# Performance work log

Hardware: AMD Instinct MI355X
Metric: run time of the kernel (lower is better)

The kernel has to match this reference:

```python
import jax, jax.numpy as jnp
import numpy as np
from jax import lax

FORGET_BIAS = 1.0
EPS = 1e-12


def l2_normalize_time(x):
    # tf.nn.l2_normalize(x, dim=1): normalize over the timestep axis
    sq = jnp.sum(jnp.square(x), axis=1, keepdims=True)
    return x * lax.rsqrt(jnp.maximum(sq, EPS))


def lstm_layer(x, W, b, units):
    """TF LSTMCell: kernel (in+units, 4*units), gates split as i, j, f, o.
    x: [B, T, D] -> [B, T, units]"""
    B = x.shape[0]

    def step(carry, xt):
        c, h = carry
        z = jnp.concatenate([xt, h], axis=-1) @ W + b  # [B, 4*units]
        i, j, f, o = jnp.split(z, 4, axis=-1)
        c = jax.nn.sigmoid(f + FORGET_BIAS) * c + jax.nn.sigmoid(i) * jnp.tanh(j)
        h = jax.nn.sigmoid(o) * jnp.tanh(c)
        return (c, h), h

    init = (jnp.zeros((B, units), x.dtype), jnp.zeros((B, units), x.dtype))
    _, hs = lax.scan(step, init, jnp.swapaxes(x, 0, 1))  # [T, B, units]
    return jnp.swapaxes(hs, 0, 1)


def setup_inputs() -> dict:
    key = jax.random.key(0)
    ks = jax.random.split(key, 5)
    B, T, U = 256, 2048, 64
    x = jax.random.normal(ks[0], (B, T, 1), dtype=jnp.float32)
    # layer 0: LSTMCell(64), input dim 1 -> kernel (1+64, 4*64)
    W0 = jax.random.normal(ks[1], (1 + U, 4 * U), dtype=jnp.float32) * 0.05
    b0 = jnp.zeros((4 * U,), dtype=jnp.float32)
    # layer 1: LSTMCell(1), input dim 64 -> kernel (64+1, 4)
    W1 = jax.random.normal(ks[2], (U + 1, 4), dtype=jnp.float32) * 0.05
    b1 = jnp.zeros((4,), dtype=jnp.float32)
    # dense(1)
    Wd = jax.random.normal(ks[3], (1, 1), dtype=jnp.float32)
    bd = jnp.zeros((1,), dtype=jnp.float32)
    return {"x": x, "W0": W0, "b0": b0, "W1": W1, "b1": b1, "Wd": Wd, "bd": bd}


def reference(x, W0, b0, W1, b1, Wd, bd):
    h = l2_normalize_time(x)          # [B, T, 1]
    h = lstm_layer(h, W0, b0, 64)     # [B, T, 64]
    h = lstm_layer(h, W1, b1, 1)      # [B, T, 1]
    out = h @ Wd + bd                 # dense(1), no activation
    return out
```

## Files before the change

### kernel.cpp

```cpp
#include <hip/hip_runtime.h>
#include <math.h>

#define TT 2048
#define UU 64
#define BB 256
#define NTHR 320

typedef float v2f __attribute__((ext_vector_type(2)));
typedef float v4f __attribute__((ext_vector_type(4)));

__device__ __forceinline__ float frcp(float x) { return __builtin_amdgcn_rcpf(x); }
__device__ __forceinline__ float fsigmoid(float x) { return frcp(1.0f + __expf(-x)); }
__device__ __forceinline__ float ftanh(float x) { return 1.0f - 2.0f * frcp(1.0f + __expf(2.0f * x)); }

__device__ __forceinline__ void pkfma(v2f& a, v2f h, v2f w) {
    asm("v_pk_fma_f32 %0, %1, %2, %0" : "+v"(a) : "v"(h), "v"(w));
}

__global__
__attribute__((amdgpu_flat_work_group_size(NTHR, NTHR)))
__attribute__((amdgpu_waves_per_eu(1, 2)))
void lstm_ts_kernel(
    const float* __restrict__ x, const float* __restrict__ W0,
    const float* __restrict__ b0, const float* __restrict__ W1,
    const float* __restrict__ b1, const float* __restrict__ Wd,
    const float* __restrict__ bd, float* __restrict__ out)
{
    __shared__ __align__(16) float xbuf[TT];
    __shared__ __align__(16) float ringP[4][2][UU];
    __shared__ __align__(16) float zbuf[4 * UU];
    __shared__ float red[5];

    const int tid = threadIdx.x;
    const int wid = tid >> 6;
    const int u = tid & 63;
    const int b = blockIdx.x;
    const float* xrow = x + b * TT;
    float* outrow = out + b * TT;

    float ss = 0.f;
    for (int i = tid; i < TT; i += NTHR) {
        float v = xrow[i];
        xbuf[i] = v;
        ss += v * v;
    }
    #pragma unroll
    for (int m = 1; m < 64; m <<= 1) ss += __shfl_xor(ss, m, 64);
    if (u == 0) red[wid] = ss;
    if (wid < 4) ringP[wid][1][u] = 0.f;
    __syncthreads();

    if (wid < 4) {
        const int g = wid;
        const int c = g * 64 + u;
        const float sq = ((red[0] + red[1]) + (red[2] + red[3])) + red[4];
        const float scale = 1.0f / sqrtf(fmaxf(sq, 1e-12f));

        #define DECLW(m) v2f WP##m; { const float* r_ = W0 + (1 + 2*(m)) * 256 + c; \
            WP##m.x = r_[0]; WP##m.y = r_[256]; } \
            asm volatile("" : "+v"(WP##m));
        DECLW(0)  DECLW(1)  DECLW(2)  DECLW(3)  DECLW(4)  DECLW(5)  DECLW(6)  DECLW(7)
        DECLW(8)  DECLW(9)  DECLW(10) DECLW(11) DECLW(12) DECLW(13) DECLW(14) DECLW(15)
        DECLW(16) DECLW(17) DECLW(18) DECLW(19) DECLW(20) DECLW(21) DECLW(22) DECLW(23)
        DECLW(24) DECLW(25) DECLW(26) DECLW(27) DECLW(28) DECLW(29) DECLW(30) DECLW(31)
        #undef DECLW

        const float wx = W0[c] * scale;
        const float bc = b0[c];

        float (*myring)[UU] = ringP[g];
        float c0 = 0.f;

        for (int t = 0; t < TT; ++t) {
            const float xr = xbuf[t];
            const float* hs = myring[(t + 1) & 1];

            v2f a0, a1 = 0.f, a2 = 0.f, a3 = 0.f;
            a0.x = fmaf(xr, wx, bc); a0.y = 0.f;

            #define MAC4(m, WA, WB, A, B) { \
                v4f hv_ = *(const v4f*)(hs + 4 * (m)); \
                v2f hA_ = __builtin_shufflevector(hv_, hv_, 0, 1); \
                v2f hB_ = __builtin_shufflevector(hv_, hv_, 2, 3); \
                pkfma(A, hA_, WA); pkfma(B, hB_, WB); \
            }
            MAC4(0,  WP0,  WP1,  a0, a1) MAC4(1,  WP2,  WP3,  a2, a3)
            MAC4(2,  WP4,  WP5,  a0, a1) MAC4(3,  WP6,  WP7,  a2, a3)
            MAC4(4,  WP8,  WP9,  a0, a1) MAC4(5,  WP10, WP11, a2, a3)
            MAC4(6,  WP12, WP13, a0, a1) MAC4(7,  WP14, WP15, a2, a3)
            MAC4(8,  WP16, WP17, a0, a1) MAC4(9,  WP18, WP19, a2, a3)
            MAC4(10, WP20, WP21, a0, a1) MAC4(11, WP22, WP23, a2, a3)
            MAC4(12, WP24, WP25, a0, a1) MAC4(13, WP26, WP27, a2, a3)
            MAC4(14, WP28, WP29, a0, a1) MAC4(15, WP30, WP31, a2, a3)
            #undef MAC4

            const v2f sz = (a0 + a1) + (a2 + a3);
            zbuf[c] = sz.x + sz.y;
            __syncthreads();

            const float zi = zbuf[u];
            const float zj = zbuf[64 + u];
            const float zf = zbuf[128 + u];
            const float zo = zbuf[192 + u];
            c0 = fsigmoid(zf + 1.0f) * c0 + fsigmoid(zi) * ftanh(zj);
            const float h = fsigmoid(zo) * ftanh(c0);

            myring[t & 1][u] = h;
        }
        __syncthreads();
    } else {
        const float w1v0 = W1[u * 4 + 0], w1v1 = W1[u * 4 + 1];
        const float w1v2 = W1[u * 4 + 2], w1v3 = W1[u * 4 + 3];
        const float w1h0 = W1[256], w1h1 = W1[257], w1h2 = W1[258], w1h3 = W1[259];
        const float b10 = b1[0], b11 = b1[1], b12 = b1[2], b13 = b1[3];
        const float wd = Wd[0], bdv = bd[0];

        float c1 = 0.f, h1 = 0.f, oval = 0.f;

        #define L1STEP(s) { \
            const float hu = ringP[0][(s) & 1][u];   \
            float p0 = hu * w1v0, p1 = hu * w1v1, p2 = hu * w1v2, p3 = hu * w1v3; \
            _Pragma("unroll") \
            for (int m = 1; m < 64; m <<= 1) { \
                p0 += __shfl_xor(p0, m, 64); \
                p1 += __shfl_xor(p1, m, 64); \
                p2 += __shfl_xor(p2, m, 64); \
                p3 += __shfl_xor(p3, m, 64); \
            } \
            const float z1i = p0 + fmaf(h1, w1h0, b10); \
            const float z1j = p1 + fmaf(h1, w1h1, b11); \
            const float z1f = p2 + fmaf(h1, w1h2, b12); \
            const float z1o = p3 + fmaf(h1, w1h3, b13); \
            c1 = fsigmoid(z1f + 1.0f) * c1 + fsigmoid(z1i) * ftanh(z1j); \
            h1 = fsigmoid(z1o) * ftanh(c1); \
            const float ov = fmaf(h1, wd, bdv); \
            if (((s) & 63) == u) oval = ov; \
            if (((s) & 63) == 63) outrow[((s) & ~63) + u] = oval; \
        }

        for (int t = 0; t < TT; ++t) {
            __syncthreads();
            if (t > 0) L1STEP(t - 1)
        }
        __syncthreads();
        L1STEP(TT - 1)
        #undef L1STEP
    }
}

extern "C" void kernel_launch(void* const* d_in, const int* in_sizes, int n_in,
                              void* d_out, int out_size, void* d_ws, size_t ws_size,
                              hipStream_t stream) {
    const float* x  = (const float*)d_in[0];
    const float* W0 = (const float*)d_in[1];
    const float* b0 = (const float*)d_in[2];
    const float* W1 = (const float*)d_in[3];
    const float* b1 = (const float*)d_in[4];
    const float* Wd = (const float*)d_in[5];
    const float* bd = (const float*)d_in[6];
    float* out = (float*)d_out;
    lstm_ts_kernel<<<BB, NTHR, 0, stream>>>(x, W0, b0, W1, b1, Wd, bd, out);
}
```

Measured before the change: 1.179 ms.

## Merge LSTM layers into four waves with in-wave gate exchange via shuffles

Drops the dedicated layer-1 wave. Each wave now owns 16 hidden units and holds all four of their gate columns, so the gates are exchanged with cross-lane shuffles instead of a shared zbuf and an extra barrier. Layer 1's input projection is done as a 16-lane shuffle reduction whose per-wave partial sums go into a 4-deep LDS ring, and the layer-1 cell update runs two steps behind in every wave. This cuts barriers per step from two to one and removes a wave, at the cost of more shuffle work and redundant layer-1 math in every wave.

Result: slower. 1.845 ms (+56.5%).

```diff
diff --git a/kernel.cpp b/kernel.cpp
--- a/kernel.cpp
+++ b/kernel.cpp
@@ -4,7 +4,7 @@
 #define TT 2048
 #define UU 64
 #define BB 256
-#define NTHR 320
+#define NTHR 256
 
 typedef float v2f __attribute__((ext_vector_type(2)));
 typedef float v4f __attribute__((ext_vector_type(4)));
@@ -17,9 +17,16 @@
     asm("v_pk_fma_f32 %0, %1, %2, %0" : "+v"(a) : "v"(h), "v"(w));
 }
 
+__device__ __forceinline__ float sel4(float v0, float v1, float v2, float v3,
+                                      int b0g, int b1g) {
+    const float lo = b0g ? v1 : v0;
+    const float hi = b0g ? v3 : v2;
+    return b1g ? hi : lo;
+}
+
 __global__
 __attribute__((amdgpu_flat_work_group_size(NTHR, NTHR)))
-__attribute__((amdgpu_waves_per_eu(1, 2)))
+__attribute__((amdgpu_waves_per_eu(1, 1)))
 void lstm_ts_kernel(
     const float* __restrict__ x, const float* __restrict__ W0,
     const float* __restrict__ b0, const float* __restrict__ W1,
@@ -27,13 +34,17 @@
     const float* __restrict__ bd, float* __restrict__ out)
 {
     __shared__ __align__(16) float xbuf[TT];
-    __shared__ __align__(16) float ringP[4][2][UU];
-    __shared__ __align__(16) float zbuf[4 * UU];
-    __shared__ float red[5];
+    __shared__ __align__(16) float ring[2][UU];
+    __shared__ __align__(16) v4f  pbuf[4][4];
+    __shared__ float red[4];
 
     const int tid = threadIdx.x;
     const int wid = tid >> 6;
-    const int u = tid & 63;
+    const int l   = tid & 63;
+    const int g   = l >> 4;
+    const int q   = l & 15;
+    const int unit = 16 * wid + q;
+    const int col  = g * 64 + unit;
     const int b = blockIdx.x;
     const float* xrow = x + b * TT;
     float* outrow = out + b * TT;
@@ -46,106 +57,127 @@
     }
     #pragma unroll
     for (int m = 1; m < 64; m <<= 1) ss += __shfl_xor(ss, m, 64);
-    if (u == 0) red[wid] = ss;
-    if (wid < 4) ringP[wid][1][u] = 0.f;
+    if (l == 0) red[wid] = ss;
+    if (tid < UU) ring[1][tid] = 0.f;
     __syncthreads();
 
-    if (wid < 4) {
-        const int g = wid;
-        const int c = g * 64 + u;
-        const float sq = ((red[0] + red[1]) + (red[2] + red[3])) + red[4];
-        const float scale = 1.0f / sqrtf(fmaxf(sq, 1e-12f));
+    const float sq = (red[0] + red[1]) + (red[2] + red[3]);
+    const float scale = 1.0f / sqrtf(fmaxf(sq, 1e-12f));
 
-        #define DECLW(m) v2f WP##m; { const float* r_ = W0 + (1 + 2*(m)) * 256 + c; \
-            WP##m.x = r_[0]; WP##m.y = r_[256]; } \
-            asm volatile("" : "+v"(WP##m));
-        DECLW(0)  DECLW(1)  DECLW(2)  DECLW(3)  DECLW(4)  DECLW(5)  DECLW(6)  DECLW(7)
-        DECLW(8)  DECLW(9)  DECLW(10) DECLW(11) DECLW(12) DECLW(13) DECLW(14) DECLW(15)
-        DECLW(16) DECLW(17) DECLW(18) DECLW(19) DECLW(20) DECLW(21) DECLW(22) DECLW(23)
-        DECLW(24) DECLW(25) DECLW(26) DECLW(27) DECLW(28) DECLW(29) DECLW(30) DECLW(31)
-        #undef DECLW
+    #define DECLW(m) v2f WP##m; { const float* r_ = W0 + (1 + 2*(m)) * 256 + col; \
+        WP##m.x = r_[0]; WP##m.y = r_[256]; } \
+        asm volatile("" : "+v"(WP##m));
+    DECLW(0)  DECLW(1)  DECLW(2)  DECLW(3)  DECLW(4)  DECLW(5)  DECLW(6)  DECLW(7)
+    DECLW(8)  DECLW(9)  DECLW(10) DECLW(11) DECLW(12) DECLW(13) DECLW(14) DECLW(15)
+    DECLW(16) DECLW(17) DECLW(18) DECLW(19) DECLW(20) DECLW(21) DECLW(22) DECLW(23)
+    DECLW(24) DECLW(25) DECLW(26) DECLW(27) DECLW(28) DECLW(29) DECLW(30) DECLW(31)
+    #undef DECLW
 
-        const float wx = W0[c] * scale;
-        const float bc = b0[c];
+    const float wx = W0[col] * scale;
+    const float bc = b0[col];
 
-        float (*myring)[UU] = ringP[g];
-        float c0 = 0.f;
+    const v4f w1r = *(const v4f*)&W1[unit * 4];
+    const float w1h0 = W1[256], w1h1 = W1[257], w1h2 = W1[258], w1h3 = W1[259];
+    const float b10 = b1[0], b11 = b1[1], b12 = b1[2], b13 = b1[3];
+    const float wd = Wd[0], bdv = bd[0];
 
-        for (int t = 0; t < TT; ++t) {
-            const float xr = xbuf[t];
-            const float* hs = myring[(t + 1) & 1];
+    const int b0g = g & 1, b1g = g & 2;
 
-            v2f a0, a1 = 0.f, a2 = 0.f, a3 = 0.f;
-            a0.x = fmaf(xr, wx, bc); a0.y = 0.f;
+    float c0 = 0.f, h_own = 0.f;
+    float c1 = 0.f, h1 = 0.f, oval = 0.f;
 
-            #define MAC4(m, WA, WB, A, B) { \
-                v4f hv_ = *(const v4f*)(hs + 4 * (m)); \
-                v2f hA_ = __builtin_shufflevector(hv_, hv_, 0, 1); \
-                v2f hB_ = __builtin_shufflevector(hv_, hv_, 2, 3); \
-                pkfma(A, hA_, WA); pkfma(B, hB_, WB); \
+    #define L1STEP(s, PB) { \
+        const v4f zp = ((PB)[0] + (PB)[1]) + ((PB)[2] + (PB)[3]); \
+        const float z1i = zp.x + fmaf(h1, w1h0, b10); \
+        const float z1j = zp.y + fmaf(h1, w1h1, b11); \
+        const float z1f = zp.z + fmaf(h1, w1h2, b12); \
+        const float z1o = zp.w + fmaf(h1, w1h3, b13); \
+        c1 = fsigmoid(z1f + 1.0f) * c1 + fsigmoid(z1i) * ftanh(z1j); \
+        h1 = fsigmoid(z1o) * ftanh(c1); \
+        const float ov = fmaf(h1, wd, bdv); \
+        if (((s) & 63) == l) oval = ov; \
+        if (wid == 0 && ((s) & 63) == 63) outrow[((s) & ~63) + l] = oval; \
+    }
+
+    for (int t = 0; t < TT; ++t) {
+        const float xr = xbuf[t];
+        const float* hs = ring[(t + 1) & 1];
+
+        v2f a0, a1 = 0.f, a2 = 0.f, a3 = 0.f;
+        a0.x = fmaf(xr, wx, bc); a0.y = 0.f;
+
+        #define MACP(m, WA, WB, A, B) { \
+            v4f hv_ = *(const v4f*)(hs + 4 * (m)); \
+            v2f hA_ = __builtin_shufflevector(hv_, hv_, 0, 1); \
+            v2f hB_ = __builtin_shufflevector(hv_, hv_, 2, 3); \
+            pkfma(A, hA_, WA); pkfma(B, hB_, WB); \
+        }
+        MACP(0,  WP0,  WP1,  a0, a1) MACP(1,  WP2,  WP3,  a2, a3)
+        MACP(2,  WP4,  WP5,  a0, a1) MACP(3,  WP6,  WP7,  a2, a3)
+        MACP(4,  WP8,  WP9,  a0, a1) MACP(5,  WP10, WP11, a2, a3)
+        MACP(6,  WP12, WP13, a0, a1) MACP(7,  WP14, WP15, a2, a3)
+        MACP(8,  WP16, WP17, a0, a1) MACP(9,  WP18, WP19, a2, a3)
+        MACP(10, WP20, WP21, a0, a1) MACP(11, WP22, WP23, a2, a3)
+        MACP(12, WP24, WP25, a0, a1) MACP(13, WP26, WP27, a2, a3)
+        MACP(14, WP28, WP29, a0, a1) MACP(15, WP30, WP31, a2, a3)
+        #undef MACP
+
+        const v2f sz = (a0 + a1) + (a2 + a3);
+        const float zown = sz.x + sz.y;
+
+        const float v0 = zown;
+        const float v1 = __shfl_xor(zown, 16, 64);
+        const float v2 = __shfl_xor(zown, 32, 64);
+        const float v3 = __shfl_xor(v1,   32, 64);
+        const float zi = sel4(v0, v1, v2, v3, b0g, b1g);
+        const float zj = sel4(v1, v0, v3, v2, b0g, b1g);
+        const float zf = sel4(v2, v3, v0, v1, b0g, b1g);
+        const float zo = sel4(v3, v2, v1, v0, b0g, b1g);
+
+        {
+            float px = h_own * w1r.x, py = h_own * w1r.y;
+            float pz = h_own * w1r.z, pw = h_own * w1r.w;
+            #pragma unroll
+            for (int m = 1; m < 16; m <<= 1) {
+                px += __shfl_xor(px, m, 64);
+                py += __shfl_xor(py, m, 64);
+                pz += __shfl_xor(pz, m, 64);
+                pw += __shfl_xor(pw, m, 64);
             }
-            MAC4(0,  WP0,  WP1,  a0, a1) MAC4(1,  WP2,  WP3,  a2, a3)
-            MAC4(2,  WP4,  WP5,  a0, a1) MAC4(3,  WP6,  WP7,  a2, a3)
-            MAC4(4,  WP8,  WP9,  a0, a1) MAC4(5,  WP10, WP11, a2, a3)
-            MAC4(6,  WP12, WP13, a0, a1) MAC4(7,  WP14, WP15, a2, a3)
-            MAC4(8,  WP16, WP17, a0, a1) MAC4(9,  WP18, WP19, a2, a3)
-            MAC4(10, WP20, WP21, a0, a1) MAC4(11, WP22, WP23, a2, a3)
-            MAC4(12, WP24, WP25, a0, a1) MAC4(13, WP26, WP27, a2, a3)
-            MAC4(14, WP28, WP29, a0, a1) MAC4(15, WP30, WP31, a2, a3)
-            #undef MAC4
-
-            const v2f sz = (a0 + a1) + (a2 + a3);
-            zbuf[c] = sz.x + sz.y;
-            __syncthreads();
-
-            const float zi = zbuf[u];
-            const float zj = zbuf[64 + u];
-            const float zf = zbuf[128 + u];
-            const float zo = zbuf[192 + u];
-            c0 = fsigmoid(zf + 1.0f) * c0 + fsigmoid(zi) * ftanh(zj);
-            const float h = fsigmoid(zo) * ftanh(c0);
-
-            myring[t & 1][u] = h;
-        }
-        __syncthreads();
-    } else {
-        const float w1v0 = W1[u * 4 + 0], w1v1 = W1[u * 4 + 1];
-        const float w1v2 = W1[u * 4 + 2], w1v3 = W1[u * 4 + 3];
-        const float w1h0 = W1[256], w1h1 = W1[257], w1h2 = W1[258], w1h3 = W1[259];
-        const float b10 = b1[0], b11 = b1[1], b12 = b1[2], b13 = b1[3];
-        const float wd = Wd[0], bdv = bd[0];
-
-        float c1 = 0.f, h1 = 0.f, oval = 0.f;
-
-        #define L1STEP(s) { \
-            const float hu = ringP[0][(s) & 1][u];   \
-            float p0 = hu * w1v0, p1 = hu * w1v1, p2 = hu * w1v2, p3 = hu * w1v3; \
-            _Pragma("unroll") \
-            for (int m = 1; m < 64; m <<= 1) { \
-                p0 += __shfl_xor(p0, m, 64); \
-                p1 += __shfl_xor(p1, m, 64); \
-                p2 += __shfl_xor(p2, m, 64); \
-                p3 += __shfl_xor(p3, m, 64); \
-            } \
-            const float z1i = p0 + fmaf(h1, w1h0, b10); \
-            const float z1j = p1 + fmaf(h1, w1h1, b11); \
-            const float z1f = p2 + fmaf(h1, w1h2, b12); \
-            const float z1o = p3 + fmaf(h1, w1h3, b13); \
-            c1 = fsigmoid(z1f + 1.0f) * c1 + fsigmoid(z1i) * ftanh(z1j); \
-            h1 = fsigmoid(z1o) * ftanh(c1); \
-            const float ov = fmaf(h1, wd, bdv); \
-            if (((s) & 63) == u) oval = ov; \
-            if (((s) & 63) == 63) outrow[((s) & ~63) + u] = oval; \
+            if (l == 15) {
+                v4f pp; pp.x = px; pp.y = py; pp.z = pz; pp.w = pw;
+                pbuf[t & 3][wid] = pp;
+            }
         }
 
-        for (int t = 0; t < TT; ++t) {
-            __syncthreads();
-            if (t > 0) L1STEP(t - 1)
+        c0 = fsigmoid(zf + 1.0f) * c0 + fsigmoid(zi) * ftanh(zj);
+        h_own = fsigmoid(zo) * ftanh(c0);
+        if (l < 16) ring[t & 1][unit] = h_own;
+
+        __syncthreads();
+
+        if (t >= 2) L1STEP(t - 2, pbuf[(t - 1) & 3])
+    }
+
+    L1STEP(TT - 2, pbuf[(TT - 1) & 3])
+    {
+        float px = h_own * w1r.x, py = h_own * w1r.y;
+        float pz = h_own * w1r.z, pw = h_own * w1r.w;
+        #pragma unroll
+        for (int m = 1; m < 16; m <<= 1) {
+            px += __shfl_xor(px, m, 64);
+            py += __shfl_xor(py, m, 64);
+            pz += __shfl_xor(pz, m, 64);
+            pw += __shfl_xor(pw, m, 64);
         }
-        __syncthreads();
-        L1STEP(TT - 1)
-        #undef L1STEP
+        if (l == 15) {
+            v4f pp; pp.x = px; pp.y = py; pp.z = pz; pp.w = pw;
+            pbuf[TT & 3][wid] = pp;
+        }
     }
+    __syncthreads();
+    L1STEP(TT - 1, pbuf[TT & 3])
+    #undef L1STEP
 }
 
 extern "C" void kernel_launch(void* const* d_in, const int* in_sizes, int n_in,
```

## Split layer-0 recurrence across two waves by hidden-unit halves with packed gate FMAs

Applied to the files above, without the earlier changes.

Layer 0 moves from four waves (one per gate) to two waves, each owning half of the recurrent input units and computing all four gates for all 64 units. Each wave writes its partial gate sums to a double-buffered shared array, reads the other wave's partials after one barrier, and then runs the cell update redundantly. Packed FMAs with op_sel broadcast one h value across two gate weights. The aim is fewer waves in each barrier and a cheaper per-step gate exchange, at the cost of twice the FMA work per wave and redundant activations. Block size drops to 192 threads and waves_per_eu is set to 1.

Result: faster. 959.4 us (-18.6%).

```diff
diff --git a/kernel.cpp b/kernel.cpp
--- a/kernel.cpp
+++ b/kernel.cpp
@@ -4,7 +4,7 @@
 #define TT 2048
 #define UU 64
 #define BB 256
-#define NTHR 320
+#define NTHR 192
 
 typedef float v2f __attribute__((ext_vector_type(2)));
 typedef float v4f __attribute__((ext_vector_type(4)));
@@ -13,13 +13,18 @@
 __device__ __forceinline__ float fsigmoid(float x) { return frcp(1.0f + __expf(-x)); }
 __device__ __forceinline__ float ftanh(float x) { return 1.0f - 2.0f * frcp(1.0f + __expf(2.0f * x)); }
 
-__device__ __forceinline__ void pkfma(v2f& a, v2f h, v2f w) {
-    asm("v_pk_fma_f32 %0, %1, %2, %0" : "+v"(a) : "v"(h), "v"(w));
+__device__ __forceinline__ void pkfma_ll(v2f& a, v2f h, v2f w) {
+    asm("v_pk_fma_f32 %0, %1, %2, %0 op_sel:[0,0,0] op_sel_hi:[0,1,1]"
+        : "+v"(a) : "v"(h), "v"(w));
+}
+__device__ __forceinline__ void pkfma_hh(v2f& a, v2f h, v2f w) {
+    asm("v_pk_fma_f32 %0, %1, %2, %0 op_sel:[1,0,0] op_sel_hi:[1,1,1]"
+        : "+v"(a) : "v"(h), "v"(w));
 }
 
 __global__
 __attribute__((amdgpu_flat_work_group_size(NTHR, NTHR)))
-__attribute__((amdgpu_waves_per_eu(1, 2)))
+__attribute__((amdgpu_waves_per_eu(1, 1)))
 void lstm_ts_kernel(
     const float* __restrict__ x, const float* __restrict__ W0,
     const float* __restrict__ b0, const float* __restrict__ W1,
@@ -27,9 +32,9 @@
     const float* __restrict__ bd, float* __restrict__ out)
 {
     __shared__ __align__(16) float xbuf[TT];
-    __shared__ __align__(16) float ringP[4][2][UU];
-    __shared__ __align__(16) float zbuf[4 * UU];
-    __shared__ float red[5];
+    __shared__ __align__(16) float ringP[2][2][UU];
+    __shared__ __align__(16) v4f  zpart[2][2][UU];
+    __shared__ float red[3];
 
     const int tid = threadIdx.x;
     const int wid = tid >> 6;
@@ -47,65 +52,76 @@
     #pragma unroll
     for (int m = 1; m < 64; m <<= 1) ss += __shfl_xor(ss, m, 64);
     if (u == 0) red[wid] = ss;
-    if (wid < 4) ringP[wid][1][u] = 0.f;
+    if (wid < 2) ringP[wid][1][u] = 0.f;
     __syncthreads();
 
-    if (wid < 4) {
-        const int g = wid;
-        const int c = g * 64 + u;
-        const float sq = ((red[0] + red[1]) + (red[2] + red[3])) + red[4];
+    if (wid < 2) {
+        const int koff = 32 * wid;
+        const float sq = (red[0] + red[1]) + red[2];
         const float scale = 1.0f / sqrtf(fmaxf(sq, 1e-12f));
 
-        #define DECLW(m) v2f WP##m; { const float* r_ = W0 + (1 + 2*(m)) * 256 + c; \
-            WP##m.x = r_[0]; WP##m.y = r_[256]; } \
-            asm volatile("" : "+v"(WP##m));
+        #define DECLW(k) v2f WI##k, WF##k; { \
+            const float* r_ = W0 + (1 + koff + (k)) * 256; \
+            WI##k.x = r_[u];       WI##k.y = r_[64 + u]; \
+            WF##k.x = r_[128 + u]; WF##k.y = r_[192 + u]; } \
+            asm volatile("" : "+v"(WI##k)); asm volatile("" : "+v"(WF##k));
         DECLW(0)  DECLW(1)  DECLW(2)  DECLW(3)  DECLW(4)  DECLW(5)  DECLW(6)  DECLW(7)
         DECLW(8)  DECLW(9)  DECLW(10) DECLW(11) DECLW(12) DECLW(13) DECLW(14) DECLW(15)
         DECLW(16) DECLW(17) DECLW(18) DECLW(19) DECLW(20) DECLW(21) DECLW(22) DECLW(23)
         DECLW(24) DECLW(25) DECLW(26) DECLW(27) DECLW(28) DECLW(29) DECLW(30) DECLW(31)
         #undef DECLW
 
-        const float wx = W0[c] * scale;
-        const float bc = b0[c];
+        const float sel = (wid == 0) ? 1.f : 0.f;
+        const float wxi = W0[u] * scale * sel,       wxj = W0[64 + u] * scale * sel;
+        const float wxf = W0[128 + u] * scale * sel, wxo = W0[192 + u] * scale * sel;
+        const float bci = b0[u] * sel,       bcj = b0[64 + u] * sel;
+        const float bcf = b0[128 + u] * sel, bco = b0[192 + u] * sel;
 
-        float (*myring)[UU] = ringP[g];
         float c0 = 0.f;
 
         for (int t = 0; t < TT; ++t) {
             const float xr = xbuf[t];
-            const float* hs = myring[(t + 1) & 1];
+            const float* hs = &ringP[wid][(t + 1) & 1][koff];
 
-            v2f a0, a1 = 0.f, a2 = 0.f, a3 = 0.f;
-            a0.x = fmaf(xr, wx, bc); a0.y = 0.f;
+            v2f ai0, ai1 = 0.f, af0, af1 = 0.f;
+            ai0.x = fmaf(xr, wxi, bci); ai0.y = fmaf(xr, wxj, bcj);
+            af0.x = fmaf(xr, wxf, bcf); af0.y = fmaf(xr, wxo, bco);
 
-            #define MAC4(m, WA, WB, A, B) { \
+            #define MACR(m, A, B, C, D, E, F, G, H) { \
                 v4f hv_ = *(const v4f*)(hs + 4 * (m)); \
-                v2f hA_ = __builtin_shufflevector(hv_, hv_, 0, 1); \
-                v2f hB_ = __builtin_shufflevector(hv_, hv_, 2, 3); \
-                pkfma(A, hA_, WA); pkfma(B, hB_, WB); \
+                v2f h01_ = __builtin_shufflevector(hv_, hv_, 0, 1); \
+                v2f h23_ = __builtin_shufflevector(hv_, hv_, 2, 3); \
+                pkfma_ll(ai0, h01_, A); pkfma_ll(af0, h01_, E); \
+                pkfma_hh(ai1, h01_, B); pkfma_hh(af1, h01_, F); \
+                pkfma_ll(ai0, h23_, C); pkfma_ll(af0, h23_, G); \
+                pkfma_hh(ai1, h23_, D); pkfma_hh(af1, h23_, H); \
             }
-            MAC4(0,  WP0,  WP1,  a0, a1) MAC4(1,  WP2,  WP3,  a2, a3)
-            MAC4(2,  WP4,  WP5,  a0, a1) MAC4(3,  WP6,  WP7,  a2, a3)
-            MAC4(4,  WP8,  WP9,  a0, a1) MAC4(5,  WP10, WP11, a2, a3)
-            MAC4(6,  WP12, WP13, a0, a1) MAC4(7,  WP14, WP15, a2, a3)
-            MAC4(8,  WP16, WP17, a0, a1) MAC4(9,  WP18, WP19, a2, a3)
-            MAC4(10, WP20, WP21, a0, a1) MAC4(11, WP22, WP23, a2, a3)
-            MAC4(12, WP24, WP25, a0, a1) MAC4(13, WP26, WP27, a2, a3)
-            MAC4(14, WP28, WP29, a0, a1) MAC4(15, WP30, WP31, a2, a3)
-            #undef MAC4
+            MACR(0, WI0,  WI1,  WI2,  WI3,  WF0,  WF1,  WF2,  WF3)
+            MACR(1, WI4,  WI5,  WI6,  WI7,  WF4,  WF5,  WF6,  WF7)
+            MACR(2, WI8,  WI9,  WI10, WI11, WF8,  WF9,  WF10, WF11)
+            MACR(3, WI12, WI13, WI14, WI15, WF12, WF13, WF14, WF15)
+            MACR(4, WI16, WI17, WI18, WI19, WF16, WF17, WF18, WF19)
+            MACR(5, WI20, WI21, WI22, WI23, WF20, WF21, WF22, WF23)
+            MACR(6, WI24, WI25, WI26, WI27, WF24, WF25, WF26, WF27)
+            MACR(7, WI28, WI29, WI30, WI31, WF28, WF29, WF30, WF31)
+            #undef MACR
 
-            const v2f sz = (a0 + a1) + (a2 + a3);
-            zbuf[c] = sz.x + sz.y;
+            const v2f pij = ai0 + ai1;
+            const v2f pfo = af0 + af1;
+            v4f zp; zp.x = pij.x; zp.y = pij.y; zp.z = pfo.x; zp.w = pfo.y;
+            zpart[t & 1][wid][u] = zp;
             __syncthreads();
 
-            const float zi = zbuf[u];
-            const float zj = zbuf[64 + u];
-            const float zf = zbuf[128 + u];
-            const float zo = zbuf[192 + u];
+            const v4f zo4 = zpart[t & 1][1 - wid][u];
+            const float zi = pij.x + zo4.x;
+            const float zj = pij.y + zo4.y;
+            const float zf = pfo.x + zo4.z;
+            const float zo = pfo.y + zo4.w;
+
             c0 = fsigmoid(zf + 1.0f) * c0 + fsigmoid(zi) * ftanh(zj);
             const float h = fsigmoid(zo) * ftanh(c0);
 
-            myring[t & 1][u] = h;
+            ringP[wid][t & 1][u] = h;
         }
         __syncthreads();
     } else {
```
